# Performance work log

Hardware: AMD Instinct MI355X
Metric: run time of the kernel (lower is better)

## Reference

```python
import jax, jax.numpy as jnp
import numpy as np

D_MODEL = 512
NUM_HEADS = 8


def setup_inputs() -> dict:
    key = jax.random.key(0)
    ks = jax.random.split(key, 12)
    B, S, D = 2, 4096, D_MODEL
    scale = 1.0 / np.sqrt(D)
    inp = {
        "q": jax.random.normal(ks[0], (B, S, D), jnp.float32),
        "k": jax.random.normal(ks[1], (B, S, D), jnp.float32),
        "v": jax.random.normal(ks[2], (B, S, D), jnp.float32),
        "w_q": jax.random.normal(ks[3], (D, D), jnp.float32) * scale,
        "b_q": jax.random.normal(ks[4], (D,), jnp.float32) * scale,
        "w_k": jax.random.normal(ks[5], (D, D), jnp.float32) * scale,
        "b_k": jax.random.normal(ks[6], (D,), jnp.float32) * scale,
        "w_v": jax.random.normal(ks[7], (D, D), jnp.float32) * scale,
        "b_v": jax.random.normal(ks[8], (D,), jnp.float32) * scale,
        "w_o": jax.random.normal(ks[9], (D, D), jnp.float32) * scale,
        "b_o": jax.random.normal(ks[10], (D,), jnp.float32) * scale,
    }
    return inp


def _split_heads(x, h):
    b, s, d = x.shape
    return x.reshape(b, s, h, d // h).transpose(0, 2, 1, 3)  # [B,H,S,dk]


def reference(q, k, v, w_q, b_q, w_k, b_k, w_v, b_v, w_o, b_o):
    h = NUM_HEADS
    # Linear projections (torch Linear: x @ W.T + b)
    qh = _split_heads(q @ w_q.T + b_q, h)
    kh = _split_heads(k @ w_k.T + b_k, h)
    vh = _split_heads(v @ w_v.T + b_v, h)
    d_k = kh.shape[-1]
    scores = jnp.einsum("bhsd,bhtd->bhst", qh, kh) / jnp.sqrt(jnp.float32(d_k))
    attn = jax.nn.softmax(scores, axis=-1)  # [B,H,S,S] - materialized, as in source
    out = jnp.einsum("bhst,bhtd->bhsd", attn, vh)
    b, _, s, dk = out.shape
    out = out.transpose(0, 2, 1, 3).reshape(b, s, h * dk)
    return out @ w_o.T + b_o
```

## Files before the change

### kernel.cpp

```cpp
#include <hip/hip_runtime.h>
#include <hip/hip_bf16.h>

#define D_MODEL 512
#define NHEAD   8
#define DK      64
#define SEQ     4096
#define BATCH   2
#define NTOK    (BATCH * SEQ)

typedef __bf16 bf16;
typedef __bf16 bf16x4 __attribute__((ext_vector_type(4)));
typedef __bf16 bf16x8 __attribute__((ext_vector_type(8)));
typedef float  f32x4  __attribute__((ext_vector_type(4)));
typedef float  f32x16 __attribute__((ext_vector_type(16)));

#define MFMA16(a, b, c) __builtin_amdgcn_mfma_f32_16x16x32_bf16((a), (b), (c), 0, 0, 0)
#define MFMA32(a, b, c) __builtin_amdgcn_mfma_f32_32x32x16_bf16((a), (b), (c), 0, 0, 0)

#define QSCALE 0.18033688f

__global__ __launch_bounds__(256) void cvt_w(
    const float* __restrict__ wq, const float* __restrict__ wk,
    const float* __restrict__ wv, const float* __restrict__ wo,
    bf16* __restrict__ Wb)
{
    int i = blockIdx.x * 256 + threadIdx.x;
    int m = i >> 16;
    int g = i & 65535;
    const float* src = (m == 0) ? wq : (m == 1) ? wk : (m == 2) ? wv : wo;
    float4 x = *(const float4*)(src + (size_t)g * 4);
    bf16x4 y = {(bf16)x.x, (bf16)x.y, (bf16)x.z, (bf16)x.w};
    *(bf16x4*)(Wb + (size_t)m * D_MODEL * D_MODEL + (size_t)g * 4) = y;
}

__global__ __launch_bounds__(256, 3) void proj_qkv(
    const float* __restrict__ q, const float* __restrict__ k, const float* __restrict__ v,
    const bf16* __restrict__ Wb,
    const float* __restrict__ bq, const float* __restrict__ bk, const float* __restrict__ bv,
    bf16* __restrict__ Qh, bf16* __restrict__ Kh, bf16* __restrict__ Vt)
{
    const int p = blockIdx.z;
    const float* X    = (p == 0) ? q  : (p == 1) ? k  : v;
    const bf16*  W    = Wb + (size_t)p * D_MODEL * D_MODEL;
    const float* bias = (p == 0) ? bq : (p == 1) ? bk : bv;

    __shared__ union __align__(16) {
        struct { bf16 As[128][72]; bf16 Bs[128][72]; } g;
        bf16 T[128][136];
    } sm;

    const int m0   = blockIdx.x * 128;
    const int n0   = blockIdx.y * 128;
    const int tid  = threadIdx.x;
    const int lane = tid & 63;
    const int wave = tid >> 6;
    const int low4 = lane & 15;
    const int quad = lane >> 4;
    const int wm   = wave >> 1;
    const int wn   = wave & 1;

    int srow[8], sc4[8];
    for (int it = 0; it < 8; ++it) {
        int idx = tid + it * 256;
        srow[it] = idx >> 4;
        sc4[it]  = (idx & 15) * 4;
    }
    int br[4], bc[4];
    for (int it = 0; it < 4; ++it) {
        int idx = tid + it * 256;
        br[it] = idx >> 3;
        bc[it] = (idx & 7) * 8;
    }

    float4 gA[8];
    bf16x8 gB[4];
    for (int it = 0; it < 8; ++it)
        gA[it] = *(const float4*)(X + (size_t)(m0 + srow[it]) * D_MODEL + sc4[it]);
    for (int it = 0; it < 4; ++it)
        gB[it] = *(const bf16x8*)(W + (size_t)(n0 + br[it]) * D_MODEL + bc[it]);

    f32x4 acc[4][4];
    for (int i = 0; i < 4; ++i)
        for (int j = 0; j < 4; ++j)
            acc[i][j] = f32x4{0.f, 0.f, 0.f, 0.f};

    for (int k0 = 0; k0 < D_MODEL; k0 += 64) {
        __syncthreads();
        for (int it = 0; it < 8; ++it) {
            bf16x4 wa = {(bf16)gA[it].x, (bf16)gA[it].y, (bf16)gA[it].z, (bf16)gA[it].w};
            *(bf16x4*)&sm.g.As[srow[it]][sc4[it]] = wa;
        }
        for (int it = 0; it < 4; ++it)
            *(bf16x8*)&sm.g.Bs[br[it]][bc[it]] = gB[it];
        __syncthreads();

        if (k0 + 64 < D_MODEL) {
            for (int it = 0; it < 8; ++it)
                gA[it] = *(const float4*)(X + (size_t)(m0 + srow[it]) * D_MODEL + k0 + 64 + sc4[it]);
            for (int it = 0; it < 4; ++it)
                gB[it] = *(const bf16x8*)(W + (size_t)(n0 + br[it]) * D_MODEL + k0 + 64 + bc[it]);
        }

        for (int ks = 0; ks < 2; ++ks) {
            bf16x8 a[4], b[4];
            for (int i = 0; i < 4; ++i)
                a[i] = *(const bf16x8*)&sm.g.As[wm * 64 + i * 16 + low4][ks * 32 + quad * 8];
            for (int j = 0; j < 4; ++j)
                b[j] = *(const bf16x8*)&sm.g.Bs[wn * 64 + j * 16 + low4][ks * 32 + quad * 8];
            for (int i = 0; i < 4; ++i)
                for (int j = 0; j < 4; ++j)
                    acc[i][j] = MFMA16(a[i], b[j], acc[i][j]);
        }
    }

    if (p < 2) {
        bf16* Out = (p == 0) ? Qh : Kh;
        const float sc = (p == 0) ? QSCALE : 1.0f;
        for (int j = 0; j < 4; ++j) {
            int col = n0 + wn * 64 + j * 16 + low4;
            float bcol = bias[col];
            for (int i = 0; i < 4; ++i)
                for (int r = 0; r < 4; ++r) {
                    int row = m0 + wm * 64 + i * 16 + quad * 4 + r;
                    Out[(size_t)row * D_MODEL + col] = (bf16)((acc[i][j][r] + bcol) * sc);
                }
        }
    } else {
        __syncthreads();
        for (int j = 0; j < 4; ++j) {
            int col = n0 + wn * 64 + j * 16 + low4;
            float bcol = bias[col];
            for (int i = 0; i < 4; ++i)
                for (int r = 0; r < 4; ++r)
                    sm.T[wn * 64 + j * 16 + low4][wm * 64 + i * 16 + quad * 4 + r] =
                        (bf16)(acc[i][j][r] + bcol);
        }
        __syncthreads();
        const int bb = m0 >> 12;
        const int s0 = (m0 & 4095);
        for (int it = 0; it < 8; ++it) {
            int cc = it * 16 + (tid >> 4);
            int ml = (tid & 15) * 8;
            int col = n0 + cc;
            int hh = col >> 6, dd = col & 63;
            *(bf16x8*)&Vt[(((size_t)(bb * NHEAD + hh) * DK + dd) << 12) + s0 + ml] =
                *(const bf16x8*)&sm.T[cc][ml];
        }
    }
}

__global__ __launch_bounds__(512, 4) void attn(
    const bf16* __restrict__ Qh, const bf16* __restrict__ Kh,
    const bf16* __restrict__ Vt, bf16* __restrict__ O)
{
    __shared__ union __align__(16) {
        struct { bf16 Ks[128][72]; bf16 Vs[64][136]; } s;
        float Obuf[4][32][68];
    } sm;
    __shared__ bf16  Ps[8][32][72];
    __shared__ float Lbuf[4][32];

    const int q0   = blockIdx.x * 128;
    const int bh   = blockIdx.y;
    const int b    = bh >> 3, h = bh & 7;
    const int tid  = threadIdx.x;
    const int lane = tid & 63;
    const int wave = tid >> 6;
    const int qg   = wave >> 1;
    const int kg   = wave & 1;
    const int m32  = lane & 31;
    const int hl   = lane >> 5;

    const bf16* Kbase = Kh + (size_t)b * SEQ * D_MODEL + h * DK;
    const bf16* Vbase = Vt + (size_t)bh * DK * SEQ;

    const bf16* Qrow = Qh + (size_t)(b * SEQ + q0 + qg * 32 + m32) * D_MODEL + h * DK;
    bf16x8 qf[4];
    for (int ks = 0; ks < 4; ++ks)
        qf[ks] = *(const bf16x8*)(Qrow + ks * 16 + hl * 8);

    float l = 0.f;
    f32x16 acc[2];
    for (int i = 0; i < 16; ++i) { acc[0][i] = 0.f; acc[1][i] = 0.f; }

    int kr[2], kc[2], vr[2], vc[2];
    for (int it = 0; it < 2; ++it) {
        int c = tid + it * 512;
        kr[it] = c >> 3;  kc[it] = (c & 7) * 8;
        vr[it] = c >> 4;  vc[it] = (c & 15) * 8;
    }
    bf16x8 gk[2], gv[2];
    for (int it = 0; it < 2; ++it) {
        gk[it] = *(const bf16x8*)(Kbase + (size_t)kr[it] * D_MODEL + kc[it]);
        gv[it] = *(const bf16x8*)(Vbase + (size_t)vr[it] * SEQ + vc[it]);
    }

    for (int t0 = 0; t0 < SEQ; t0 += 128) {
        __syncthreads();
        for (int it = 0; it < 2; ++it) {
            *(bf16x8*)&sm.s.Ks[kr[it]][kc[it]] = gk[it];
            *(bf16x8*)&sm.s.Vs[vr[it]][vc[it]] = gv[it];
        }
        __syncthreads();

        if (t0 + 128 < SEQ) {
            for (int it = 0; it < 2; ++it) {
                gk[it] = *(const bf16x8*)(Kbase + (size_t)(t0 + 128 + kr[it]) * D_MODEL + kc[it]);
                gv[it] = *(const bf16x8*)(Vbase + (size_t)vr[it] * SEQ + t0 + 128 + vc[it]);
            }
        }

        for (int mt = 0; mt < 2; ++mt) {
            f32x16 sc;
            for (int i = 0; i < 16; ++i) sc[i] = 0.f;
            for (int ks = 0; ks < 4; ++ks) {
                bf16x8 kf = *(const bf16x8*)&sm.s.Ks[kg * 64 + mt * 32 + m32][ks * 16 + hl * 8];
                sc = MFMA32(kf, qf[ks], sc);
            }
            for (int g = 0; g < 4; ++g) {
                float p0 = __builtin_amdgcn_exp2f(sc[g * 4 + 0]);
                float p1 = __builtin_amdgcn_exp2f(sc[g * 4 + 1]);
                float p2 = __builtin_amdgcn_exp2f(sc[g * 4 + 2]);
                float p3 = __builtin_amdgcn_exp2f(sc[g * 4 + 3]);
                l += (p0 + p1) + (p2 + p3);
                bf16x4 pw = {(bf16)p0, (bf16)p1, (bf16)p2, (bf16)p3};
                *(bf16x4*)&Ps[wave][m32][mt * 32 + g * 8 + hl * 4] = pw;
            }
        }

        for (int ks = 0; ks < 4; ++ks) {
            bf16x8 pf = *(const bf16x8*)&Ps[wave][m32][ks * 16 + hl * 8];
            for (int nt = 0; nt < 2; ++nt) {
                bf16x8 vfr = *(const bf16x8*)&sm.s.Vs[nt * 32 + m32][kg * 64 + ks * 16 + hl * 8];
                acc[nt] = MFMA32(pf, vfr, acc[nt]);
            }
        }
    }

    l += __shfl_xor(l, 32);
    __syncthreads();
    if (kg == 1) {
        for (int nt = 0; nt < 2; ++nt)
            for (int r = 0; r < 16; ++r) {
                int qq = (r & 3) + 8 * (r >> 2) + 4 * hl;
                sm.Obuf[qg][qq][nt * 32 + m32] = acc[nt][r];
            }
        if (hl == 0) Lbuf[qg][m32] = l;
    }
    __syncthreads();
    if (kg == 0) {
        float lt  = l + Lbuf[qg][m32];
        float inv = 1.0f / lt;
        for (int nt = 0; nt < 2; ++nt)
            for (int r = 0; r < 16; ++r) {
                int qq = (r & 3) + 8 * (r >> 2) + 4 * hl;
                float val = acc[nt][r] + sm.Obuf[qg][qq][nt * 32 + m32];
                float iv  = __shfl(inv, qq);
                O[(size_t)(b * SEQ + q0 + qg * 32 + qq) * D_MODEL + h * DK + nt * 32 + m32] =
                    (bf16)(val * iv);
            }
    }
}

__global__ __launch_bounds__(256, 4) void proj_out(
    const bf16* __restrict__ Oin, const bf16* __restrict__ Wo,
    const float* __restrict__ bo, float* __restrict__ out)
{
    __shared__ bf16 As[64][72];
    __shared__ bf16 Bs[64][72];

    const int m0   = blockIdx.x * 64;
    const int n0   = blockIdx.y * 64;
    const int tid  = threadIdx.x;
    const int lane = tid & 63;
    const int wave = tid >> 6;
    const int low4 = lane & 15;
    const int quad = lane >> 4;
    const int wm   = wave >> 1;
    const int wn   = wave & 1;

    int arow[2], ag[2];
    for (int it = 0; it < 2; ++it) {
        int idx = tid + it * 256;
        arow[it] = idx >> 3;
        ag[it]   = (idx & 7) * 8;
    }

    bf16x8 gA[2], gB[2];
    for (int it = 0; it < 2; ++it) {
        gA[it] = *(const bf16x8*)(Oin + (size_t)(m0 + arow[it]) * D_MODEL + ag[it]);
        gB[it] = *(const bf16x8*)(Wo + (size_t)(n0 + arow[it]) * D_MODEL + ag[it]);
    }

    f32x4 acc[2][2];
    for (int i = 0; i < 2; ++i)
        for (int j = 0; j < 2; ++j)
            acc[i][j] = f32x4{0.f, 0.f, 0.f, 0.f};

    for (int k0 = 0; k0 < D_MODEL; k0 += 64) {
        __syncthreads();
        for (int it = 0; it < 2; ++it) {
            *(bf16x8*)&As[arow[it]][ag[it]] = gA[it];
            *(bf16x8*)&Bs[arow[it]][ag[it]] = gB[it];
        }
        __syncthreads();

        if (k0 + 64 < D_MODEL) {
            for (int it = 0; it < 2; ++it) {
                gA[it] = *(const bf16x8*)(Oin + (size_t)(m0 + arow[it]) * D_MODEL + k0 + 64 + ag[it]);
                gB[it] = *(const bf16x8*)(Wo + (size_t)(n0 + arow[it]) * D_MODEL + k0 + 64 + ag[it]);
            }
        }

        for (int ks = 0; ks < 2; ++ks) {
            bf16x8 a[2], b[2];
            for (int i = 0; i < 2; ++i)
                a[i] = *(const bf16x8*)&As[wm * 32 + i * 16 + low4][ks * 32 + quad * 8];
            for (int j = 0; j < 2; ++j)
                b[j] = *(const bf16x8*)&Bs[wn * 32 + j * 16 + low4][ks * 32 + quad * 8];
            for (int i = 0; i < 2; ++i)
                for (int j = 0; j < 2; ++j)
                    acc[i][j] = MFMA16(a[i], b[j], acc[i][j]);
        }
    }

    for (int j = 0; j < 2; ++j) {
        int col = n0 + wn * 32 + j * 16 + low4;
        float bcol = bo[col];
        for (int i = 0; i < 2; ++i)
            for (int r = 0; r < 4; ++r) {
                int row = m0 + wm * 32 + i * 16 + quad * 4 + r;
                out[(size_t)row * D_MODEL + col] = acc[i][j][r] + bcol;
            }
    }
}

extern "C" void kernel_launch(void* const* d_in, const int* in_sizes, int n_in,
                              void* d_out, int out_size, void* d_ws, size_t ws_size,
                              hipStream_t stream)
{
    const float* q  = (const float*)d_in[0];
    const float* k  = (const float*)d_in[1];
    const float* v  = (const float*)d_in[2];
    const float* wq = (const float*)d_in[3];
    const float* bq = (const float*)d_in[4];
    const float* wk = (const float*)d_in[5];
    const float* bk = (const float*)d_in[6];
    const float* wv = (const float*)d_in[7];
    const float* bv = (const float*)d_in[8];
    const float* wo = (const float*)d_in[9];
    const float* bo = (const float*)d_in[10];

    const size_t NT = (size_t)NTOK * D_MODEL;
    bf16* Qh = (bf16*)d_ws;
    bf16* Kh = Qh + NT;
    bf16* Vt = Kh + NT;
    bf16* O  = Vt + NT;
    bf16* Wb = O + NT;

    cvt_w<<<1024, 256, 0, stream>>>(wq, wk, wv, wo, Wb);

    dim3 g1(NTOK / 128, D_MODEL / 128, 3);
    proj_qkv<<<g1, 256, 0, stream>>>(q, k, v, Wb, bq, bk, bv, Qh, Kh, Vt);

    dim3 g2(SEQ / 128, BATCH * NHEAD);
    attn<<<g2, 512, 0, stream>>>(Qh, Kh, Vt, O);

    dim3 g3(NTOK / 64, D_MODEL / 64);
    proj_out<<<g3, 256, 0, stream>>>(O, Wb + (size_t)3 * D_MODEL * D_MODEL, bo, (float*)d_out);
}
```

Measured before the change: 237.9 us.

## Double-buffer K/V in swizzled LDS and pass P through registers via permlane swaps

The attention loop now keeps two XOR-swizzled LDS buffers for K and V, so each tile needs one barrier instead of two and the next tile's store overlaps the current compute. The P tile no longer goes through an LDS scratch buffer: probabilities are packed with v_cvt_pk_bf16_f32 and rearranged into MFMA A-operand layout with permlane32_swap. s_setprio is raised around the MFMA sections. The extra K/V buffer doubles that part of LDS, which may reduce occupancy, and the swizzle index maths must match the fragment reads exactly.

```diff
diff --git a/kernel.cpp b/kernel.cpp
--- a/kernel.cpp
+++ b/kernel.cpp
@@ -13,11 +13,18 @@
 typedef __bf16 bf16x8 __attribute__((ext_vector_type(8)));
 typedef float  f32x4  __attribute__((ext_vector_type(4)));
 typedef float  f32x16 __attribute__((ext_vector_type(16)));
+typedef unsigned u32x4 __attribute__((ext_vector_type(4)));
 
 #define MFMA16(a, b, c) __builtin_amdgcn_mfma_f32_16x16x32_bf16((a), (b), (c), 0, 0, 0)
 #define MFMA32(a, b, c) __builtin_amdgcn_mfma_f32_32x32x16_bf16((a), (b), (c), 0, 0, 0)
 
 #define QSCALE 0.18033688f
+
+__device__ __forceinline__ unsigned cvt_pk_bf16(float a, float b) {
+    unsigned r;
+    asm("v_cvt_pk_bf16_f32 %0, %1, %2" : "=v"(r) : "v"(a), "v"(b));
+    return r;
+}
 
 __global__ __launch_bounds__(256) void cvt_w(
     const float* __restrict__ wq, const float* __restrict__ wk,
@@ -154,10 +161,9 @@
     const bf16* __restrict__ Vt, bf16* __restrict__ O)
 {
     __shared__ union __align__(16) {
-        struct { bf16 Ks[128][72]; bf16 Vs[64][136]; } s;
+        struct { bf16 K[2][128 * 64]; bf16 V[2][64 * 128]; } s;
         float Obuf[4][32][68];
     } sm;
-    __shared__ bf16  Ps[8][32][72];
     __shared__ float Lbuf[4][32];
 
     const int q0   = blockIdx.x * 128;
@@ -170,6 +176,7 @@
     const int kg   = wave & 1;
     const int m32  = lane & 31;
     const int hl   = lane >> 5;
+    const int rb   = m32 & 7;
 
     const bf16* Kbase = Kh + (size_t)b * SEQ * D_MODEL + h * DK;
     const bf16* Vbase = Vt + (size_t)bh * DK * SEQ;
@@ -183,56 +190,93 @@
     f32x16 acc[2];
     for (int i = 0; i < 16; ++i) { acc[0][i] = 0.f; acc[1][i] = 0.f; }
 
-    int kr[2], kc[2], vr[2], vc[2];
+    int kr[2], kc[2], vr[2], vc[2], kso[2], vso[2];
     for (int it = 0; it < 2; ++it) {
         int c = tid + it * 512;
         kr[it] = c >> 3;  kc[it] = (c & 7) * 8;
         vr[it] = c >> 4;  vc[it] = (c & 15) * 8;
-    }
+        kso[it] = kr[it] * 64  + (((c & 7)  ^ (kr[it] & 7)) << 3);
+        vso[it] = vr[it] * 128 + (((c & 15) ^ (vr[it] & 7)) << 3);
+    }
+
     bf16x8 gk[2], gv[2];
     for (int it = 0; it < 2; ++it) {
         gk[it] = *(const bf16x8*)(Kbase + (size_t)kr[it] * D_MODEL + kc[it]);
         gv[it] = *(const bf16x8*)(Vbase + (size_t)vr[it] * SEQ + vc[it]);
     }
+    for (int it = 0; it < 2; ++it) {
+        *(bf16x8*)&sm.s.K[0][kso[it]] = gk[it];
+        *(bf16x8*)&sm.s.V[0][vso[it]] = gv[it];
+    }
 
     for (int t0 = 0; t0 < SEQ; t0 += 128) {
-        __syncthreads();
-        for (int it = 0; it < 2; ++it) {
-            *(bf16x8*)&sm.s.Ks[kr[it]][kc[it]] = gk[it];
-            *(bf16x8*)&sm.s.Vs[vr[it]][vc[it]] = gv[it];
-        }
-        __syncthreads();
-
-        if (t0 + 128 < SEQ) {
+        const int cur = (t0 >> 7) & 1;
+        const bf16* Kc = sm.s.K[cur];
+        const bf16* Vc = sm.s.V[cur];
+
+        const bool pf_next = (t0 + 128 < SEQ);
+        if (pf_next) {
             for (int it = 0; it < 2; ++it) {
                 gk[it] = *(const bf16x8*)(Kbase + (size_t)(t0 + 128 + kr[it]) * D_MODEL + kc[it]);
                 gv[it] = *(const bf16x8*)(Vbase + (size_t)vr[it] * SEQ + t0 + 128 + vc[it]);
             }
         }
 
+        __syncthreads();
+
         for (int mt = 0; mt < 2; ++mt) {
             f32x16 sc;
             for (int i = 0; i < 16; ++i) sc[i] = 0.f;
+            const int krow = kg * 64 + mt * 32 + m32;
+            __builtin_amdgcn_s_setprio(1);
             for (int ks = 0; ks < 4; ++ks) {
-                bf16x8 kf = *(const bf16x8*)&sm.s.Ks[kg * 64 + mt * 32 + m32][ks * 16 + hl * 8];
+                bf16x8 kf = *(const bf16x8*)&Kc[krow * 64 + (((ks * 2 + hl) ^ rb) << 3)];
                 sc = MFMA32(kf, qf[ks], sc);
             }
+            __builtin_amdgcn_s_setprio(0);
+
+            unsigned x[8];
             for (int g = 0; g < 4; ++g) {
                 float p0 = __builtin_amdgcn_exp2f(sc[g * 4 + 0]);
                 float p1 = __builtin_amdgcn_exp2f(sc[g * 4 + 1]);
                 float p2 = __builtin_amdgcn_exp2f(sc[g * 4 + 2]);
                 float p3 = __builtin_amdgcn_exp2f(sc[g * 4 + 3]);
                 l += (p0 + p1) + (p2 + p3);
-                bf16x4 pw = {(bf16)p0, (bf16)p1, (bf16)p2, (bf16)p3};
-                *(bf16x4*)&Ps[wave][m32][mt * 32 + g * 8 + hl * 4] = pw;
-            }
-        }
-
-        for (int ks = 0; ks < 4; ++ks) {
-            bf16x8 pf = *(const bf16x8*)&Ps[wave][m32][ks * 16 + hl * 8];
+                x[2 * g]     = cvt_pk_bf16(p0, p1);
+                x[2 * g + 1] = cvt_pk_bf16(p2, p3);
+            }
+
+            u32x4 pa, pb;
+            {
+                auto s0 = __builtin_amdgcn_permlane32_swap(x[0], x[2], false, false);
+                pa[0] = s0[0]; pa[2] = s0[1];
+                auto s1 = __builtin_amdgcn_permlane32_swap(x[1], x[3], false, false);
+                pa[1] = s1[0]; pa[3] = s1[1];
+                auto s2 = __builtin_amdgcn_permlane32_swap(x[4], x[6], false, false);
+                pb[0] = s2[0]; pb[2] = s2[1];
+                auto s3 = __builtin_amdgcn_permlane32_swap(x[5], x[7], false, false);
+                pb[1] = s3[0]; pb[3] = s3[1];
+            }
+            bf16x8 pfa = __builtin_bit_cast(bf16x8, pa);
+            bf16x8 pfb = __builtin_bit_cast(bf16x8, pb);
+
+            __builtin_amdgcn_s_setprio(1);
             for (int nt = 0; nt < 2; ++nt) {
-                bf16x8 vfr = *(const bf16x8*)&sm.s.Vs[nt * 32 + m32][kg * 64 + ks * 16 + hl * 8];
-                acc[nt] = MFMA32(pf, vfr, acc[nt]);
+                const int vrow = nt * 32 + m32;
+                bf16x8 va = *(const bf16x8*)&Vc[vrow * 128 + (((kg * 8 + (2 * mt) * 2 + hl) ^ rb) << 3)];
+                acc[nt] = MFMA32(pfa, va, acc[nt]);
+                bf16x8 vb = *(const bf16x8*)&Vc[vrow * 128 + (((kg * 8 + (2 * mt + 1) * 2 + hl) ^ rb) << 3)];
+                acc[nt] = MFMA32(pfb, vb, acc[nt]);
+            }
+            __builtin_amdgcn_s_setprio(0);
+        }
+
+        if (pf_next) {
+            bf16* Kn = sm.s.K[cur ^ 1];
+            bf16* Vn = sm.s.V[cur ^ 1];
+            for (int it = 0; it < 2; ++it) {
+                *(bf16x8*)&Kn[kso[it]] = gk[it];
+                *(bf16x8*)&Vn[vso[it]] = gv[it];
             }
         }
     }
```

Measured after the change: 240.3 us. Within noise of the previous version (+1.0%).
